# Kernel optimization log

Hardware: AMD Instinct MI355X
Metric: run time of the kernel (lower is better)

Reference implementation:

```python
import jax, jax.numpy as jnp
import numpy as np

B, N, F = 1024, 784, 1
C1, C2, H, NCLS = 32, 32, 512, 10


def setup_inputs() -> dict:
    key = jax.random.key(0)
    ks = jax.random.split(key, 10)
    x = jax.random.normal(ks[0], (B, N, F), jnp.float32)
    # dense (renormalized-style) adjacency, shared across the batch; rows roughly sum to ~1
    a = jax.random.uniform(ks[1], (N, N), jnp.float32) * (2.0 / N)
    def glorot(k, shape):
        lim = np.sqrt(6.0 / (shape[0] + shape[1])).astype(np.float32)
        return jax.random.uniform(k, shape, jnp.float32, -lim, lim)
    return {
        "x": x,
        "a": a,
        "w1": glorot(ks[2], (F, C1)),
        "b1": jnp.zeros((C1,), jnp.float32),
        "w2": glorot(ks[3], (C1, C2)),
        "b2": jnp.zeros((C2,), jnp.float32),
        "wf1": glorot(ks[4], (N * C2, H)),
        "bf1": jnp.zeros((H,), jnp.float32),
        "wf2": glorot(ks[5], (H, NCLS)),
        "bf2": jnp.zeros((NCLS,), jnp.float32),
    }


def _graph_conv(x, a, w, b):
    # Spektral GraphConv (batch mode): elu(A @ (X @ W) + b)
    xw = jnp.einsum('bnf,fc->bnc', x, w)
    agg = jnp.einsum('nm,bmc->bnc', a, xw)
    return jax.nn.elu(agg + b)


def reference(x, a, w1, b1, w2, b2, wf1, bf1, wf2, bf2):
    h = _graph_conv(x, a, w1, b1)          # [B, N, 32]
    h = _graph_conv(h, a, w2, b2)          # [B, N, 32]
    h = h.reshape(h.shape[0], -1)          # Flatten -> [B, N*32]
    h = jax.nn.relu(h @ wf1 + bf1)         # [B, 512]
    return jax.nn.softmax(h @ wf2 + bf2, axis=-1)  # [B, 10]
```

## Files before the change

### kernel.cpp

```cpp
#include <hip/hip_runtime.h>
#include <hip/hip_bf16.h>
#include <math.h>

#define BATCH 1024
#define NREAL 784
#define NPAD  896
#define C1D   32
#define C2D   32
#define HDIM  512
#define NCLS  10
#define KFC   25088

#define KS_G1 7
#define KS_FC 14

#define BM 128
#define BN 128
#define BK 32

using bf16x8  = __attribute__((ext_vector_type(8))) __bf16;
using floatx4 = __attribute__((ext_vector_type(4))) float;

__device__ __forceinline__ float elu_f(float t) {
    return t > 0.f ? t : (__expf(t) - 1.f);
}

__device__ __forceinline__ void wg_barrier_lds() {
    asm volatile("s_waitcnt lgkmcnt(0)\n\ts_barrier" ::: "memory");
}

__device__ __forceinline__ void bar() {
    asm volatile("s_barrier" ::: "memory");
}

__device__ __forceinline__ void gload_lds16(const __hip_bfloat16* g, __hip_bfloat16* l) {
    __builtin_amdgcn_global_load_lds(
        (const __attribute__((address_space(1))) void*)g,
        (__attribute__((address_space(3))) void*)l, 16, 0, 0);
}

template<int MODE>
__launch_bounds__(256)
__global__ void gemm_bt(const __hip_bfloat16* __restrict__ A, int lda,
                        const __hip_bfloat16* __restrict__ Bm, int ldb,
                        int kIters, int kPerZ, size_t sliceStride,
                        float* __restrict__ outF, int ldc,
                        __hip_bfloat16* __restrict__ outH,
                        const float* __restrict__ bias)
{
    __shared__ __align__(16) __hip_bfloat16 As[2][BM * BK];
    __shared__ __align__(16) __hip_bfloat16 Bs[2][BN * BK];

    const int tid  = threadIdx.x;
    const int lane = tid & 63;
    const int wave = tid >> 6;
    const int wi = wave >> 1, wj = wave & 1;

    const int m0 = blockIdx.y * BM;
    const int n0 = blockIdx.x * BN;
    const int kBase = blockIdx.z * kPerZ;

    const int rowInChunk = lane >> 2;
    const int kOff8 = (lane & 3) * 8;

    const __hip_bfloat16* aSrc0 = A  + (size_t)(m0 + (wave * 2 + 0) * 16 + rowInChunk) * lda + kBase + kOff8;
    const __hip_bfloat16* aSrc1 = A  + (size_t)(m0 + (wave * 2 + 1) * 16 + rowInChunk) * lda + kBase + kOff8;
    const __hip_bfloat16* bSrc0 = Bm + (size_t)(n0 + (wave * 2 + 0) * 16 + rowInChunk) * ldb + kBase + kOff8;
    const __hip_bfloat16* bSrc1 = Bm + (size_t)(n0 + (wave * 2 + 1) * 16 + rowInChunk) * ldb + kBase + kOff8;

    const int wSlot = (((lane & 3) + ((lane >> 3) & 3)) & 3) * 8;
    const int ldsW0 = (wave * 2 + 0) * 512 + rowInChunk * 32 + wSlot;
    const int ldsW1 = ldsW0 + 512;

    const int rSlot = ((((lane >> 4) + (((lane & 15) >> 1) & 3)) & 3)) * 8;
    const int rRow  = lane & 15;

    floatx4 acc[4][4];
    const floatx4 zero4 = {0.f, 0.f, 0.f, 0.f};
    #pragma unroll
    for (int i = 0; i < 4; i++)
        #pragma unroll
        for (int j = 0; j < 4; j++) acc[i][j] = zero4;

    int4 aA0, aA1, bA0, bA1;
    int4 aB0, aB1, bB0, bB1;

    aA0 = *(const int4*)aSrc0; aA1 = *(const int4*)aSrc1;
    bA0 = *(const int4*)bSrc0; bA1 = *(const int4*)bSrc1;
    aSrc0 += BK; aSrc1 += BK; bSrc0 += BK; bSrc1 += BK;
    aB0 = *(const int4*)aSrc0; aB1 = *(const int4*)aSrc1;
    bB0 = *(const int4*)bSrc0; bB1 = *(const int4*)bSrc1;
    aSrc0 += BK; aSrc1 += BK; bSrc0 += BK; bSrc1 += BK;

    *(int4*)(&As[0][ldsW0]) = aA0;
    *(int4*)(&As[0][ldsW1]) = aA1;
    *(int4*)(&Bs[0][ldsW0]) = bA0;
    *(int4*)(&Bs[0][ldsW1]) = bA1;
    wg_barrier_lds();

    for (int kt = 0; kt < kIters; kt += 2) {
        const bool more = (kt + 2 < kIters);

        {
            bf16x8 af[4], bfr[4];
            #pragma unroll
            for (int mi = 0; mi < 4; mi++)
                af[mi] = *(const bf16x8*)(&As[0][(wi * 64 + mi * 16 + rRow) * BK + rSlot]);
            #pragma unroll
            for (int nj = 0; nj < 4; nj++)
                bfr[nj] = *(const bf16x8*)(&Bs[0][(wj * 64 + nj * 16 + rRow) * BK + rSlot]);

            if (more) {
                aA0 = *(const int4*)aSrc0; aA1 = *(const int4*)aSrc1;
                bA0 = *(const int4*)bSrc0; bA1 = *(const int4*)bSrc1;
                aSrc0 += BK; aSrc1 += BK; bSrc0 += BK; bSrc1 += BK;
            }
            *(int4*)(&As[1][ldsW0]) = aB0;
            *(int4*)(&As[1][ldsW1]) = aB1;
            *(int4*)(&Bs[1][ldsW0]) = bB0;
            *(int4*)(&Bs[1][ldsW1]) = bB1;

            #pragma unroll
            for (int mi = 0; mi < 4; mi++)
                #pragma unroll
                for (int nj = 0; nj < 4; nj++)
                    acc[mi][nj] = __builtin_amdgcn_mfma_f32_16x16x32_bf16(af[mi], bfr[nj], acc[mi][nj], 0, 0, 0);

            wg_barrier_lds();
        }

        {
            bf16x8 af[4], bfr[4];
            #pragma unroll
            for (int mi = 0; mi < 4; mi++)
                af[mi] = *(const bf16x8*)(&As[1][(wi * 64 + mi * 16 + rRow) * BK + rSlot]);
            #pragma unroll
            for (int nj = 0; nj < 4; nj++)
                bfr[nj] = *(const bf16x8*)(&Bs[1][(wj * 64 + nj * 16 + rRow) * BK + rSlot]);

            if (more) {
                aB0 = *(const int4*)aSrc0; aB1 = *(const int4*)aSrc1;
                bB0 = *(const int4*)bSrc0; bB1 = *(const int4*)bSrc1;
                aSrc0 += BK; aSrc1 += BK; bSrc0 += BK; bSrc1 += BK;
                *(int4*)(&As[0][ldsW0]) = aA0;
                *(int4*)(&As[0][ldsW1]) = aA1;
                *(int4*)(&Bs[0][ldsW0]) = bA0;
                *(int4*)(&Bs[0][ldsW1]) = bA1;
            }

            #pragma unroll
            for (int mi = 0; mi < 4; mi++)
                #pragma unroll
                for (int nj = 0; nj < 4; nj++)
                    acc[mi][nj] = __builtin_amdgcn_mfma_f32_16x16x32_bf16(af[mi], bfr[nj], acc[mi][nj], 0, 0, 0);

            wg_barrier_lds();
        }
    }

    #pragma unroll
    for (int mi = 0; mi < 4; mi++) {
        #pragma unroll
        for (int nj = 0; nj < 4; nj++) {
            #pragma unroll
            for (int r = 0; r < 4; r++) {
                const int row = m0 + wi * 64 + mi * 16 + (lane >> 4) * 4 + r;
                const int col = n0 + wj * 64 + nj * 16 + (lane & 15);
                const float v = acc[mi][nj][r];
                if (MODE == 1) {
                    if (row < NREAL) {
                        const int c = col & 31, b = col >> 5;
                        const float t = elu_f(v + bias[c]);
                        outH[(size_t)b * KFC + row * 32 + c] = __float2bfloat16(t);
                    }
                } else {
                    outF[(size_t)blockIdx.z * sliceStride + (size_t)row * ldc + col] = v;
                }
            }
        }
    }
}

#define KT_G3 14

#define STAGE_A(tt, hh) do {                                                    \
    const int s_ = (2 * (tt) + (hh)) & 3;                                       \
    gload_lds16(aSrcH[hh][0] + (tt) * 64, &Ah[s_][(wave * 2 + 0) * 512]);       \
    gload_lds16(aSrcH[hh][1] + (tt) * 64, &Ah[s_][(wave * 2 + 1) * 512]);       \
} while (0)

#define STAGE_B(tt, hh) do {                                                    \
    const int s_ = (2 * (tt) + (hh)) & 3;                                       \
    gload_lds16(bSrcH[hh][0] + (tt) * 64, &Bh[s_][(wave * 2 + 0) * 512]);       \
    gload_lds16(bSrcH[hh][1] + (tt) * 64, &Bh[s_][(wave * 2 + 1) * 512]);       \
} while (0)

__launch_bounds__(512, 2)
__global__ void gemm256_g3(const __hip_bfloat16* __restrict__ Ag,
                           const __hip_bfloat16* __restrict__ Bg,
                           __hip_bfloat16* __restrict__ outH,
                           const float* __restrict__ bias)
{
    __shared__ __align__(16) __hip_bfloat16 Ah[4][128 * 64];
    __shared__ __align__(16) __hip_bfloat16 Bh[4][128 * 64];

    const int tid  = threadIdx.x;
    const int lane = tid & 63;
    const int wave = tid >> 6;
    const int vm = wave >> 2, vn = wave & 3;
    const int hbB = vn >> 1;

    const int mR = blockIdx.y * 256;
    const int nR = blockIdx.x * 256;

    const int rRow = lane & 15;
    const int gHi  = lane >> 4;
    const int rot  = lane & 7;
    const int koff0 = (((gHi + rot) & 7) << 3);
    const int koff1 = ((((gHi + 4) + rot) & 7) << 3);
    const int aRow0 = rRow * 64;
    const int bRow0 = ((vn & 1) * 64 + rRow) * 64;

    const int rowLoc = lane >> 3;
    const int gOff   = ((((lane & 7) - rowLoc) & 7) << 3);
    const __hip_bfloat16* aSrcH[2][2];
    const __hip_bfloat16* bSrcH[2][2];
    #pragma unroll
    for (int h = 0; h < 2; h++)
        #pragma unroll
        for (int j = 0; j < 2; j++) {
            int ra = mR + h * 128 + (wave * 2 + j) * 8 + rowLoc;
            if (ra > NPAD - 1) ra = NPAD - 1;
            aSrcH[h][j] = Ag + (size_t)ra * NPAD + gOff;
            const int rb = nR + h * 128 + (wave * 2 + j) * 8 + rowLoc;
            bSrcH[h][j] = Bg + (size_t)rb * NPAD + gOff;
        }

    const float bias0 = bias[rRow];
    const float bias1 = bias[16 + rRow];

    floatx4 acc[8][4];
    const floatx4 zero4 = {0.f, 0.f, 0.f, 0.f};
    #pragma unroll
    for (int i = 0; i < 8; i++)
        #pragma unroll
        for (int j = 0; j < 4; j++) acc[i][j] = zero4;

    STAGE_A(0, 0); STAGE_A(0, 1);
    STAGE_B(0, 0); STAGE_B(0, 1);

    #pragma unroll 2
    for (int t = 0; t < KT_G3; ++t) {
        asm volatile("s_waitcnt vmcnt(0)" ::: "memory");
        bar();

        const int sA = (2 * t + vm)  & 3;
        const int sB = (2 * t + hbB) & 3;
        const __hip_bfloat16* Ab = &Ah[sA][aRow0];
        const __hip_bfloat16* Bb = &Bh[sB][bRow0];

        bf16x8 a_[4], b_[4];

        #pragma unroll
        for (int nj = 0; nj < 4; nj++) b_[nj] = *(const bf16x8*)(Bb + nj * 1024 + koff0);
        #pragma unroll
        for (int mi = 0; mi < 4; mi++) a_[mi] = *(const bf16x8*)(Ab + mi * 1024 + koff0);
        if (t + 1 < KT_G3) { STAGE_A(t + 1, 0); STAGE_A(t + 1, 1); }
        __builtin_amdgcn_s_setprio(1);
        #pragma unroll
        for (int mi = 0; mi < 4; mi++)
            #pragma unroll
            for (int nj = 0; nj < 4; nj++)
                acc[mi][nj] = __builtin_amdgcn_mfma_f32_16x16x32_bf16(a_[mi], b_[nj], acc[mi][nj], 0, 0, 0);
        __builtin_amdgcn_s_setprio(0);

        #pragma unroll
        for (int mi = 0; mi < 4; mi++) a_[mi] = *(const bf16x8*)(Ab + (4 + mi) * 1024 + koff0);
        if (t + 1 < KT_G3) { STAGE_B(t + 1, 0); STAGE_B(t + 1, 1); }
        __builtin_amdgcn_s_setprio(1);
        #pragma unroll
        for (int mi = 0; mi < 4; mi++)
            #pragma unroll
            for (int nj = 0; nj < 4; nj++)
                acc[4 + mi][nj] = __builtin_amdgcn_mfma_f32_16x16x32_bf16(a_[mi], b_[nj], acc[4 + mi][nj], 0, 0, 0);
        __builtin_amdgcn_s_setprio(0);

        #pragma unroll
        for (int nj = 0; nj < 4; nj++) b_[nj] = *(const bf16x8*)(Bb + nj * 1024 + koff1);
        #pragma unroll
        for (int mi = 0; mi < 4; mi++) a_[mi] = *(const bf16x8*)(Ab + mi * 1024 + koff1);
        __builtin_amdgcn_s_setprio(1);
        #pragma unroll
        for (int mi = 0; mi < 4; mi++)
            #pragma unroll
            for (int nj = 0; nj < 4; nj++)
                acc[mi][nj] = __builtin_amdgcn_mfma_f32_16x16x32_bf16(a_[mi], b_[nj], acc[mi][nj], 0, 0, 0);
        __builtin_amdgcn_s_setprio(0);

        #pragma unroll
        for (int mi = 0; mi < 4; mi++) a_[mi] = *(const bf16x8*)(Ab + (4 + mi) * 1024 + koff1);
        __builtin_amdgcn_s_setprio(1);
        #pragma unroll
        for (int mi = 0; mi < 4; mi++)
            #pragma unroll
            for (int nj = 0; nj < 4; nj++)
                acc[4 + mi][nj] = __builtin_amdgcn_mfma_f32_16x16x32_bf16(a_[mi], b_[nj], acc[4 + mi][nj], 0, 0, 0);
        __builtin_amdgcn_s_setprio(0);
    }

    #pragma unroll
    for (int mi = 0; mi < 8; mi++) {
        #pragma unroll
        for (int nj = 0; nj < 4; nj++) {
            #pragma unroll
            for (int r = 0; r < 4; r++) {
                const int row = mR + vm * 128 + mi * 16 + gHi * 4 + r;
                if (row < NREAL) {
                    const int col = nR + vn * 64 + nj * 16 + rRow;
                    const int c = col & 31, b = col >> 5;
                    const float bv = (nj & 1) ? bias1 : bias0;
                    const float v = elu_f(acc[mi][nj][r] + bv);
                    outH[(size_t)b * KFC + row * 32 + c] = __float2bfloat16(v);
                }
            }
        }
    }
}

__global__ void convX(const float* __restrict__ x, __hip_bfloat16* __restrict__ Xbf) {
    const int idx = blockIdx.x * 256 + threadIdx.x;
    if (idx >= BATCH * NPAD) return;
    const int m = idx % NPAD, b = idx / NPAD;
    const float v = (m < NREAL) ? x[(size_t)b * NREAL + m] : 0.f;
    Xbf[idx] = __float2bfloat16(v);
}

__global__ void convA(const float* __restrict__ a, __hip_bfloat16* __restrict__ Abf) {
    const int idx = blockIdx.x * 256 + threadIdx.x;
    if (idx >= NPAD * NPAD) return;
    const int m = idx % NPAD, n = idx / NPAD;
    const float v = (m < NREAL && n < NREAL) ? a[(size_t)n * NREAL + m] : 0.f;
    Abf[idx] = __float2bfloat16(v);
}

__global__ void convW(const float* __restrict__ wf1, __hip_bfloat16* __restrict__ Wt) {
    __shared__ float tile[32][33];
    const int k0 = blockIdx.x * 32, h0 = blockIdx.y * 32;
    const int tx = threadIdx.x, ty = threadIdx.y;
    #pragma unroll
    for (int i = 0; i < 4; i++)
        tile[ty * 4 + i][tx] = wf1[(size_t)(k0 + ty * 4 + i) * HDIM + h0 + tx];
    __syncthreads();
    #pragma unroll
    for (int i = 0; i < 4; i++)
        Wt[(size_t)(h0 + ty * 4 + i) * KFC + k0 + tx] = __float2bfloat16(tile[tx][ty * 4 + i]);
}

__global__ void layer1_fuse(const float* __restrict__ Ypart,
                            const float* __restrict__ w1, const float* __restrict__ b1,
                            const float* __restrict__ w2,
                            __hip_bfloat16* __restrict__ Tt)
{
    __shared__ __align__(16) float sW2[C1D * C2D];
    __shared__ float sw1[C1D], sb1[C1D];
    const int tid = threadIdx.x;
    for (int i = tid; i < C1D * C2D; i += 128) sW2[i] = w2[i];
    if (tid < C1D) { sw1[tid] = w1[tid]; sb1[tid] = b1[tid]; }
    __syncthreads();

    const int m = blockIdx.x * 128 + tid;
    const int b = blockIdx.y;
    float y = 0.f;
    #pragma unroll
    for (int z = 0; z < KS_G1; z++)
        y += Ypart[(size_t)z * (BATCH * NPAD) + (size_t)b * NPAD + m];

    float h[C1D];
    #pragma unroll
    for (int c1 = 0; c1 < C1D; c1++) h[c1] = elu_f(y * sw1[c1] + sb1[c1]);

    float4 t4[8];
    #pragma unroll
    for (int q = 0; q < 8; q++) t4[q] = make_float4(0.f, 0.f, 0.f, 0.f);
    #pragma unroll
    for (int c1 = 0; c1 < C1D; c1++) {
        const float hv = h[c1];
        const float4* row = (const float4*)(sW2 + c1 * C2D);
        #pragma unroll
        for (int q = 0; q < 8; q++) {
            const float4 w = row[q];
            t4[q].x += hv * w.x; t4[q].y += hv * w.y;
            t4[q].z += hv * w.z; t4[q].w += hv * w.w;
        }
    }
    const float* tf = (const float*)t4;
    #pragma unroll
    for (int c = 0; c < C2D; c++)
        Tt[((size_t)(b * 32 + c)) * NPAD + m] = __float2bfloat16(tf[c]);
}

__global__ void fc2_softmax(const float* __restrict__ part, const float* __restrict__ bf1,
                            const float* __restrict__ wf2, const float* __restrict__ bf2,
                            float* __restrict__ out)
{
    __shared__ float sW[HDIM * NCLS];
    __shared__ float sb[NCLS];
    const int tid = threadIdx.x;
    for (int i = tid; i < HDIM * NCLS; i += 256) sW[i] = wf2[i];
    if (tid < NCLS) sb[tid] = bf2[tid];
    __syncthreads();

    const int lane = tid & 63, wave = tid >> 6;
    const int b = blockIdx.x * 4 + wave;

    float acc[NCLS];
    #pragma unroll
    for (int c = 0; c < NCLS; c++) acc[c] = 0.f;
    #pragma unroll
    for (int q = 0; q < 8; q++) {
        const int h = q * 64 + lane;
        float hv = bf1[h];
        #pragma unroll
        for (int z = 0; z < KS_FC; z++)
            hv += part[(size_t)z * (BATCH * HDIM) + (size_t)b * HDIM + h];
        hv = hv > 0.f ? hv : 0.f;
        #pragma unroll
        for (int c = 0; c < NCLS; c++) acc[c] += hv * sW[h * NCLS + c];
    }
    #pragma unroll
    for (int c = 0; c < NCLS; c++) {
        #pragma unroll
        for (int off = 32; off >= 1; off >>= 1) acc[c] += __shfl_down(acc[c], off);
    }
    if (lane == 0) {
        float mx = -1e30f;
        #pragma unroll
        for (int c = 0; c < NCLS; c++) { acc[c] += sb[c]; mx = fmaxf(mx, acc[c]); }
        float e[NCLS], s = 0.f;
        #pragma unroll
        for (int c = 0; c < NCLS; c++) { e[c] = __expf(acc[c] - mx); s += e[c]; }
        const float inv = 1.f / s;
        #pragma unroll
        for (int c = 0; c < NCLS; c++) out[(size_t)b * NCLS + c] = e[c] * inv;
    }
}

extern "C" void kernel_launch(void* const* d_in, const int* in_sizes, int n_in,
                              void* d_out, int out_size, void* d_ws, size_t ws_size,
                              hipStream_t stream)
{
    const float* x   = (const float*)d_in[0];
    const float* a   = (const float*)d_in[1];
    const float* w1  = (const float*)d_in[2];
    const float* b1  = (const float*)d_in[3];
    const float* w2  = (const float*)d_in[4];
    const float* b2  = (const float*)d_in[5];
    const float* wf1 = (const float*)d_in[6];
    const float* bf1 = (const float*)d_in[7];
    const float* wf2 = (const float*)d_in[8];
    const float* bf2 = (const float*)d_in[9];
    float* out = (float*)d_out;

    char* ws = (char*)d_ws;
    __hip_bfloat16* h2f  = (__hip_bfloat16*)(ws + 0);
    float*          Ypart= (float*)(ws + 0);
    __hip_bfloat16* Tt   = (__hip_bfloat16*)(ws + 51380224);
    __hip_bfloat16* Wt   = (__hip_bfloat16*)(ws + 51380224);
    float*          part = (float*)(ws + 77070336);
    __hip_bfloat16* Abf  = (__hip_bfloat16*)(ws + 110100480);
    __hip_bfloat16* Xbf  = (__hip_bfloat16*)(ws + 111706112);

    convX<<<(BATCH * NPAD + 255) / 256, 256, 0, stream>>>(x, Xbf);
    convA<<<(NPAD * NPAD + 255) / 256, 256, 0, stream>>>(a, Abf);

    gemm_bt<2><<<dim3(NPAD / BN, BATCH / BM, KS_G1), 256, 0, stream>>>(
        Xbf, NPAD, Abf, NPAD, (NPAD / KS_G1) / BK, NPAD / KS_G1,
        (size_t)BATCH * NPAD, Ypart, NPAD, nullptr, nullptr);

    layer1_fuse<<<dim3(NPAD / 128, BATCH), 128, 0, stream>>>(Ypart, w1, b1, w2, Tt);

    gemm256_g3<<<dim3(BATCH * 32 / 256, 1024 / 256), 512, 0, stream>>>(Abf, Tt, h2f, b2);

    convW<<<dim3(KFC / 32, HDIM / 32), dim3(32, 8), 0, stream>>>(wf1, Wt);

    gemm_bt<2><<<dim3(HDIM / BN, BATCH / BM, KS_FC), 256, 0, stream>>>(
        h2f, KFC, Wt, KFC, (KFC / KS_FC) / BK, KFC / KS_FC,
        (size_t)BATCH * HDIM, part, HDIM, nullptr, nullptr);

    fc2_softmax<<<BATCH / 4, 256, 0, stream>>>(part, bf1, wf2, bf2, out);
}
```

Measured before the change: 295.7 us.

## Restructure 256x256 GEMM into quadrant-wise compute with deeper half-tile prefetch

Reworks the gemm256_g3 main loop so each wave owns a 64x32 sub-tile in each of four 128x128 quadrants. The loop consumes A/B half-tiles in quadrant order and interleaves global-to-LDS staging of the next half-tiles, prefetching one extra half-tile ahead. It waits with vmcnt(4) instead of vmcnt(0) so loads stay in flight across the barrier. The aim is to overlap memory latency with MFMA work and reduce full drains, at the cost of an extra mid-iteration barrier, a different LDS read pattern and more complex stage bookkeeping.

```diff
diff --git a/kernel.cpp b/kernel.cpp
--- a/kernel.cpp
+++ b/kernel.cpp
@@ -208,7 +208,6 @@
     const int lane = tid & 63;
     const int wave = tid >> 6;
     const int vm = wave >> 2, vn = wave & 3;
-    const int hbB = vn >> 1;
 
     const int mR = blockIdx.y * 256;
     const int nR = blockIdx.x * 256;
@@ -218,8 +217,8 @@
     const int rot  = lane & 7;
     const int koff0 = (((gHi + rot) & 7) << 3);
     const int koff1 = ((((gHi + 4) + rot) & 7) << 3);
-    const int aRow0 = rRow * 64;
-    const int bRow0 = ((vn & 1) * 64 + rRow) * 64;
+    const int aBase = (vm * 64 + rRow) * 64;
+    const int bBase = (vn * 32 + rRow) * 64;
 
     const int rowLoc = lane >> 3;
     const int gOff   = ((((lane & 7) - rowLoc) & 7) << 3);
@@ -239,88 +238,129 @@
     const float bias0 = bias[rRow];
     const float bias1 = bias[16 + rRow];
 
-    floatx4 acc[8][4];
+    floatx4 acc[4][4][2];
     const floatx4 zero4 = {0.f, 0.f, 0.f, 0.f};
     #pragma unroll
-    for (int i = 0; i < 8; i++)
-        #pragma unroll
-        for (int j = 0; j < 4; j++) acc[i][j] = zero4;
-
-    STAGE_A(0, 0); STAGE_A(0, 1);
-    STAGE_B(0, 0); STAGE_B(0, 1);
+    for (int q = 0; q < 4; q++)
+        #pragma unroll
+        for (int i = 0; i < 4; i++)
+            #pragma unroll
+            for (int j = 0; j < 2; j++) acc[q][i][j] = zero4;
+
+    STAGE_A(0, 0); STAGE_B(0, 1);
+    STAGE_A(0, 1); STAGE_B(0, 0);
+    STAGE_A(1, 0); STAGE_B(1, 1);
 
     #pragma unroll 2
     for (int t = 0; t < KT_G3; ++t) {
-        asm volatile("s_waitcnt vmcnt(0)" ::: "memory");
+        if (t + 1 < KT_G3) { asm volatile("s_waitcnt vmcnt(4)" ::: "memory"); }
+        else               { asm volatile("s_waitcnt vmcnt(0)" ::: "memory"); }
         bar();
 
-        const int sA = (2 * t + vm)  & 3;
-        const int sB = (2 * t + hbB) & 3;
-        const __hip_bfloat16* Ab = &Ah[sA][aRow0];
-        const __hip_bfloat16* Bb = &Bh[sB][bRow0];
-
-        bf16x8 a_[4], b_[4];
-
-        #pragma unroll
-        for (int nj = 0; nj < 4; nj++) b_[nj] = *(const bf16x8*)(Bb + nj * 1024 + koff0);
-        #pragma unroll
-        for (int mi = 0; mi < 4; mi++) a_[mi] = *(const bf16x8*)(Ab + mi * 1024 + koff0);
-        if (t + 1 < KT_G3) { STAGE_A(t + 1, 0); STAGE_A(t + 1, 1); }
+        const int sA0 = (2 * t + 0) & 3, sA1 = (2 * t + 1) & 3;
+        const int sB0 = (2 * t + 0) & 3, sB1 = (2 * t + 1) & 3;
+
+        bf16x8 aF[4][2], bF[2][2];
+
+        #pragma unroll
+        for (int mi = 0; mi < 4; mi++) {
+            aF[mi][0] = *(const bf16x8*)(&Ah[sA0][aBase + mi * 1024 + koff0]);
+            aF[mi][1] = *(const bf16x8*)(&Ah[sA0][aBase + mi * 1024 + koff1]);
+        }
+        #pragma unroll
+        for (int nj = 0; nj < 2; nj++) {
+            bF[nj][0] = *(const bf16x8*)(&Bh[sB0][bBase + nj * 1024 + koff0]);
+            bF[nj][1] = *(const bf16x8*)(&Bh[sB0][bBase + nj * 1024 + koff1]);
+        }
+        if (t + 1 < KT_G3) { STAGE_A(t + 1, 1); STAGE_B(t + 1, 0); }
         __builtin_amdgcn_s_setprio(1);
         #pragma unroll
         for (int mi = 0; mi < 4; mi++)
             #pragma unroll
-            for (int nj = 0; nj < 4; nj++)
-                acc[mi][nj] = __builtin_amdgcn_mfma_f32_16x16x32_bf16(a_[mi], b_[nj], acc[mi][nj], 0, 0, 0);
+            for (int nj = 0; nj < 2; nj++)
+                acc[0][mi][nj] = __builtin_amdgcn_mfma_f32_16x16x32_bf16(aF[mi][0], bF[nj][0], acc[0][mi][nj], 0, 0, 0);
+        #pragma unroll
+        for (int mi = 0; mi < 4; mi++)
+            #pragma unroll
+            for (int nj = 0; nj < 2; nj++)
+                acc[0][mi][nj] = __builtin_amdgcn_mfma_f32_16x16x32_bf16(aF[mi][1], bF[nj][1], acc[0][mi][nj], 0, 0, 0);
         __builtin_amdgcn_s_setprio(0);
 
         #pragma unroll
-        for (int mi = 0; mi < 4; mi++) a_[mi] = *(const bf16x8*)(Ab + (4 + mi) * 1024 + koff0);
-        if (t + 1 < KT_G3) { STAGE_B(t + 1, 0); STAGE_B(t + 1, 1); }
+        for (int nj = 0; nj < 2; nj++) {
+            bF[nj][0] = *(const bf16x8*)(&Bh[sB1][bBase + nj * 1024 + koff0]);
+            bF[nj][1] = *(const bf16x8*)(&Bh[sB1][bBase + nj * 1024 + koff1]);
+        }
         __builtin_amdgcn_s_setprio(1);
         #pragma unroll
         for (int mi = 0; mi < 4; mi++)
             #pragma unroll
-            for (int nj = 0; nj < 4; nj++)
-                acc[4 + mi][nj] = __builtin_amdgcn_mfma_f32_16x16x32_bf16(a_[mi], b_[nj], acc[4 + mi][nj], 0, 0, 0);
+            for (int nj = 0; nj < 2; nj++)
+                acc[1][mi][nj] = __builtin_amdgcn_mfma_f32_16x16x32_bf16(aF[mi][0], bF[nj][0], acc[1][mi][nj], 0, 0, 0);
+        #pragma unroll
+        for (int mi = 0; mi < 4; mi++)
+            #pragma unroll
+            for (int nj = 0; nj < 2; nj++)
+                acc[1][mi][nj] = __builtin_amdgcn_mfma_f32_16x16x32_bf16(aF[mi][1], bF[nj][1], acc[1][mi][nj], 0, 0, 0);
         __builtin_amdgcn_s_setprio(0);
 
-        #pragma unroll
-        for (int nj = 0; nj < 4; nj++) b_[nj] = *(const bf16x8*)(Bb + nj * 1024 + koff1);
-        #pragma unroll
-        for (int mi = 0; mi < 4; mi++) a_[mi] = *(const bf16x8*)(Ab + mi * 1024 + koff1);
+        bar();
+
+        #pragma unroll
+        for (int mi = 0; mi < 4; mi++) {
+            aF[mi][0] = *(const bf16x8*)(&Ah[sA1][aBase + mi * 1024 + koff0]);
+            aF[mi][1] = *(const bf16x8*)(&Ah[sA1][aBase + mi * 1024 + koff1]);
+        }
+        if (t + 2 < KT_G3) { STAGE_A(t + 2, 0); STAGE_B(t + 2, 1); }
         __builtin_amdgcn_s_setprio(1);
         #pragma unroll
         for (int mi = 0; mi < 4; mi++)
             #pragma unroll
-            for (int nj = 0; nj < 4; nj++)
-                acc[mi][nj] = __builtin_amdgcn_mfma_f32_16x16x32_bf16(a_[mi], b_[nj], acc[mi][nj], 0, 0, 0);
+            for (int nj = 0; nj < 2; nj++)
+                acc[3][mi][nj] = __builtin_amdgcn_mfma_f32_16x16x32_bf16(aF[mi][0], bF[nj][0], acc[3][mi][nj], 0, 0, 0);
+        #pragma unroll
+        for (int mi = 0; mi < 4; mi++)
+            #pragma unroll
+            for (int nj = 0; nj < 2; nj++)
+                acc[3][mi][nj] = __builtin_amdgcn_mfma_f32_16x16x32_bf16(aF[mi][1], bF[nj][1], acc[3][mi][nj], 0, 0, 0);
         __builtin_amdgcn_s_setprio(0);
 
         #pragma unroll
-        for (int mi = 0; mi < 4; mi++) a_[mi] = *(const bf16x8*)(Ab + (4 + mi) * 1024 + koff1);
+        for (int nj = 0; nj < 2; nj++) {
+            bF[nj][0] = *(const bf16x8*)(&Bh[sB0][bBase + nj * 1024 + koff0]);
+            bF[nj][1] = *(const bf16x8*)(&Bh[sB0][bBase + nj * 1024 + koff1]);
+        }
         __builtin_amdgcn_s_setprio(1);
         #pragma unroll
         for (int mi = 0; mi < 4; mi++)
             #pragma unroll
-            for (int nj = 0; nj < 4; nj++)
-                acc[4 + mi][nj] = __builtin_amdgcn_mfma_f32_16x16x32_bf16(a_[mi], b_[nj], acc[4 + mi][nj], 0, 0, 0);
+            for (int nj = 0; nj < 2; nj++)
+                acc[2][mi][nj] = __builtin_amdgcn_mfma_f32_16x16x32_bf16(aF[mi][0], bF[nj][0], acc[2][mi][nj], 0, 0, 0);
+        #pragma unroll
+        for (int mi = 0; mi < 4; mi++)
+            #pragma unroll
+            for (int nj = 0; nj < 2; nj++)
+                acc[2][mi][nj] = __builtin_amdgcn_mfma_f32_16x16x32_bf16(aF[mi][1], bF[nj][1], acc[2][mi][nj], 0, 0, 0);
         __builtin_amdgcn_s_setprio(0);
     }
 
     #pragma unroll
-    for (int mi = 0; mi < 8; mi++) {
-        #pragma unroll
-        for (int nj = 0; nj < 4; nj++) {
-            #pragma unroll
-            for (int r = 0; r < 4; r++) {
-                const int row = mR + vm * 128 + mi * 16 + gHi * 4 + r;
-                if (row < NREAL) {
-                    const int col = nR + vn * 64 + nj * 16 + rRow;
-                    const int c = col & 31, b = col >> 5;
-                    const float bv = (nj & 1) ? bias1 : bias0;
-                    const float v = elu_f(acc[mi][nj][r] + bv);
-                    outH[(size_t)b * KFC + row * 32 + c] = __float2bfloat16(v);
+    for (int q = 0; q < 4; q++) {
+        const int qm = q >> 1, qn = q & 1;
+        #pragma unroll
+        for (int mi = 0; mi < 4; mi++) {
+            #pragma unroll
+            for (int nj = 0; nj < 2; nj++) {
+                #pragma unroll
+                for (int r = 0; r < 4; r++) {
+                    const int row = mR + qm * 128 + vm * 64 + mi * 16 + gHi * 4 + r;
+                    if (row < NREAL) {
+                        const int col = nR + qn * 128 + vn * 32 + nj * 16 + rRow;
+                        const int c = col & 31, b = col >> 5;
+                        const float bv = nj ? bias1 : bias0;
+                        const float v = elu_f(acc[q][mi][nj][r] + bv);
+                        outH[(size_t)b * KFC + row * 32 + c] = __float2bfloat16(v);
+                    }
                 }
             }
         }
```

New measurement: 273.3 us. 7.6% less time.
